# Performance work log

Hardware: AMD Instinct MI355X
Metric: run time of the kernel (lower is better)

The kernel has to match this reference:

```python
import jax, jax.numpy as jnp
import numpy as np

N_NOTES = 4096
SIZE = 64
N_EDGE_TYPE = 14  # len(GRAPH_KEYS) * 2
N_ITER = 5


def setup_inputs() -> dict:
    key = jax.random.key(0)
    ks = jax.random.split(key, 12)
    xav = np.sqrt(2.0 / (SIZE + SIZE))  # xavier_normal_ std for square [SIZE,SIZE]
    x = jax.random.normal(ks[0], (N_NOTES, SIZE), dtype=jnp.float32)
    # sparse binary adjacency per edge type (avg degree ~8) to keep gate
    # pre-activations in a sane range, as a real score graph would be
    edge_matrix = (jax.random.uniform(ks[1], (N_EDGE_TYPE, N_NOTES, N_NOTES)) < 0.002).astype(jnp.float32)
    wz = jax.random.normal(ks[2], (N_EDGE_TYPE, SIZE, SIZE), dtype=jnp.float32) * xav
    wr = jax.random.normal(ks[3], (N_EDGE_TYPE, SIZE, SIZE), dtype=jnp.float32) * xav
    wh = jax.random.normal(ks[4], (N_EDGE_TYPE, SIZE, SIZE), dtype=jnp.float32) * xav
    uz = jax.random.normal(ks[5], (SIZE, SIZE), dtype=jnp.float32) * xav
    ur = jax.random.normal(ks[6], (SIZE, SIZE), dtype=jnp.float32) * xav
    uh = jax.random.normal(ks[7], (SIZE, SIZE), dtype=jnp.float32) * xav
    bz = jnp.zeros((SIZE,), dtype=jnp.float32)
    br = jnp.zeros((SIZE,), dtype=jnp.float32)
    bh = jnp.zeros((SIZE,), dtype=jnp.float32)
    return {"x": x, "edge_matrix": edge_matrix, "wz": wz, "wr": wr, "wh": wh,
            "uz": uz, "ur": ur, "uh": uh, "bz": bz, "br": br, "bh": bh}


def reference(x, edge_matrix, wz, wr, wh, uz, ur, uh, bz, br, bh):
    # Faithful GatedGraph.forward: 5 iterations of edge-typed message passing
    # with GRU-style gates and the (unusual, but as-written) blend
    #   h <- (1 - z) * h + r * h_tilde
    h = x  # [N, D]
    for _ in range(N_ITER):
        # activation[e, n, d] = sum_m edge[e, m, n] * h[m, d]  (edge_matrix.transpose(1,2) @ h)
        act = jnp.einsum('emn,md->end', edge_matrix, h)  # [E, N, D]
        az = jnp.einsum('end,edf->nf', act, wz)  # bmm(act, wz).sum(0)
        ar = jnp.einsum('end,edf->nf', act, wr)
        ah = jnp.einsum('end,edf->nf', act, wh)
        z = jax.nn.sigmoid(az + h @ uz + bz)
        r = jax.nn.sigmoid(ar + h @ ur + br)
        h_tilde = jnp.tanh(ah + (r * h) @ uh + bh)
        h = (1.0 - z) * h + r * h_tilde
    return h
```

## Files before the change

kernel.cpp:

```cpp
#include <hip/hip_runtime.h>
#include <hip/hip_bf16.h>
#include <cstdint>

#define N_NOTES 4096
#define SIZE 64
#define NE 14
#define NITER 5
#define MAXDEG 64
#define KTOT 960
#define ASTR 968
#define HPAD 4113
#define PWN 184320
#define PUN 4096
#define PSTR 264

typedef __attribute__((ext_vector_type(8))) short short8;
typedef __attribute__((ext_vector_type(4))) float float4v;

__device__ __forceinline__ ushort f2bf(float f){
  union{float f; uint32_t u;} x; x.f=f;
  uint32_t r = x.u + 0x7fffu + ((x.u>>16)&1u);
  return (ushort)(r>>16);
}
__device__ __forceinline__ float bf2f(ushort h){
  union{uint32_t u; float f;} x; x.u=((uint32_t)h)<<16; return x.f;
}
__device__ __forceinline__ void split_bf(float v, ushort& hi, ushort& lo){
  hi = f2bf(v);
  lo = f2bf(v - bf2f(hi));
}

__global__ __launch_bounds__(256) void k_zero(int* __restrict__ deg, uint32_t* __restrict__ adj32,
                                              float* __restrict__ h0pad, float* __restrict__ h1pad){
  int i = blockIdx.x*256 + threadIdx.x;
  if (i < NE*N_NOTES) deg[i] = 0;
  for (int j = i; j < NE*N_NOTES*MAXDEG/2; j += gridDim.x*256)
    adj32[j] = 0x10101010u;
  if (i < (HPAD-N_NOTES)*SIZE){ h0pad[i] = 0.f; h1pad[i] = 0.f; }
}

__global__ __launch_bounds__(256) void k_build(const float4v* __restrict__ edge4,
                                               int* __restrict__ deg,
                                               ushort* __restrict__ adj){
  int row = blockIdx.x;
  int e = row >> 12, m = row & 4095;
  const float4v* p = edge4 + (size_t)row * (N_NOTES/4);
  int t = threadIdx.x;
  #pragma unroll
  for (int i=0;i<4;i++){
    int idx4 = t + i*256;
    float4v v = p[idx4];
    int nbase = idx4*4;
    #pragma unroll
    for (int j=0;j<4;j++){
      if (v[j] != 0.0f){
        int n = nbase + j;
        int slot = atomicAdd(&deg[(e<<12)+n], 1);
        if (slot < MAXDEG) adj[(size_t)((e<<12)+n)*MAXDEG + slot] = (ushort)m;
      }
    }
  }
}

__global__ __launch_bounds__(256) void k_pack(const float* __restrict__ wz, const float* __restrict__ wr,
                                              const float* __restrict__ wh, const float* __restrict__ uz,
                                              const float* __restrict__ ur, const float* __restrict__ uh,
                                              ushort* __restrict__ PWH, ushort* __restrict__ PWL,
                                              ushort* __restrict__ PUH, ushort* __restrict__ PUL){
  int idx = blockIdx.x*256 + threadIdx.x;
  if (idx < PWN){
    int j = idx & 7, lane = (idx>>3)&63, t = idx>>9;
    int kk = t % 30, wg = t/30; int cb = wg & 3, g = wg >> 2;
    int col = g*64 + cb*16 + (lane&15);
    int k = kk*32 + ((lane>>4)<<3) + j;
    int e = k >> 6, d = k & 63, f = col & 63;
    float v;
    if (e < NE){
      const float* wp = (g==0)?wz:(g==1)?wr:wh;
      v = wp[(e*64 + d)*64 + f];
    } else {
      v = (g==0) ? uz[d*64+f] : (g==1) ? ur[d*64+f] : 0.0f;
    }
    ushort hi,lo; split_bf(v,hi,lo);
    PWH[idx]=hi; PWL[idx]=lo;
  } else if (idx < PWN + PUN){
    int i2 = idx - PWN;
    int j = i2 & 7, lane = (i2>>3)&63, t = i2>>9;
    int kk = t & 1, cb = t >> 1;
    int col = cb*16 + (lane&15);
    int k = kk*32 + ((lane>>4)<<3) + j;
    float v = uh[k*64 + col];
    ushort hi,lo; split_bf(v,hi,lo);
    PUH[i2]=hi; PUL[i2]=lo;
  }
}

__global__ __launch_bounds__(1024, 4)
void k_fused(const int* __restrict__ deg, const ushort* __restrict__ adj,
             const ushort* __restrict__ PWH, const ushort* __restrict__ PWL,
             const ushort* __restrict__ PUH, const ushort* __restrict__ PUL,
             const float* __restrict__ bz, const float* __restrict__ br,
             const float* __restrict__ bh,
             const float* __restrict__ hin, float* __restrict__ hout,
             float* __restrict__ out, int last){
  __shared__ ushort sh[31744];
  ushort* aHs = sh;
  ushort* aLs = sh + 16*ASTR;
  float*  PSf = (float*)sh;
  ushort* rhH = sh + 25344;
  ushort* rhL = sh + 26496;
  float*  zSf = (float*)(sh + 27648);
  float*  rSf = (float*)(sh + 29696);

  const int tid  = threadIdx.x;
  const int w    = tid >> 6;
  const int lane = tid & 63;
  const int qi   = lane >> 4;
  const int ql   = lane & 15;
  const int l15  = lane & 15;
  const int koff = (lane >> 4) * 8;
  const int r0   = blockIdx.x * 16;
  const float4v* hin4 = (const float4v*)hin;

  const int Q = w*4 + qi;
  int dgv[4], mvv[4];
  #pragma unroll
  for (int p=0;p<4;p++){
    int u = p*64 + Q;
    int e = u >> 4, n = r0 + (u & 15);
    if (e < NE){
      int base = (e<<12) + n;
      dgv[p] = deg[base];
      mvv[p] = adj[(size_t)base*MAXDEG + ql];
    } else { dgv[p]=0; mvv[p]=0; }
  }
  #pragma unroll
  for (int p=0;p<4;p++){
    int u = p*64 + Q;
    if (u >= 240) continue;
    int e = u >> 4, ri = u & 15, n = r0 + ri;
    float4v a0={0.f,0.f,0.f,0.f}, a1={0.f,0.f,0.f,0.f};
    float4v a2={0.f,0.f,0.f,0.f}, a3={0.f,0.f,0.f,0.f};
    if (e < NE){
      #pragma unroll
      for (int k=0;k<16;k+=4){
        int m0 = __shfl(mvv[p], qi*16 + k);
        int m1 = __shfl(mvv[p], qi*16 + k+1);
        int m2 = __shfl(mvv[p], qi*16 + k+2);
        int m3 = __shfl(mvv[p], qi*16 + k+3);
        a0 += hin4[m0*16 + ql];
        a1 += hin4[m1*16 + ql];
        a2 += hin4[m2*16 + ql];
        a3 += hin4[m3*16 + ql];
      }
      int dg = dgv[p];
      if (dg > 16){
        size_t base = (size_t)((e<<12)+n)*MAXDEG;
        for (int k=16;k<dg;k++){
          int m = adj[base + k];
          a0 += hin4[m*16 + ql];
        }
      }
    } else {
      a0 = hin4[n*16 + ql];
    }
    float4v acc = (a0 + a1) + (a2 + a3);
    ushort h0,h1,h2,h3,l0,l1,l2,l3;
    split_bf(acc[0],h0,l0); split_bf(acc[1],h1,l1);
    split_bf(acc[2],h2,l2); split_bf(acc[3],h3,l3);
    int o = ri*ASTR + e*64 + ql*4;
    *(ushort4*)&aHs[o] = make_ushort4(h0,h1,h2,h3);
    *(ushort4*)&aLs[o] = make_ushort4(l0,l1,l2,l3);
  }
  __syncthreads();

  const int cb = w & 3, kq = w >> 2;
  const int kk0 = kq*8;
  float4v acc[3];
  #pragma unroll
  for (int g=0;g<3;g++) acc[g] = (float4v){0.f,0.f,0.f,0.f};
  #pragma unroll
  for (int kx=0; kx<8; ++kx){
    int kk = kk0 + kx;
    if (kk < 30){
      short8 aH = *(const short8*)&aHs[l15*ASTR + kk*32 + koff];
      short8 aL = *(const short8*)&aLs[l15*ASTR + kk*32 + koff];
      #pragma unroll
      for (int g=0; g<3; ++g){
        int boff = (((g*4 + cb)*30 + kk) << 9) + lane*8;
        short8 bH = *(const short8*)(PWH + boff);
        short8 bL = *(const short8*)(PWL + boff);
        acc[g] = __builtin_amdgcn_mfma_f32_16x16x32_bf16(aH,bH,acc[g],0,0,0);
        acc[g] = __builtin_amdgcn_mfma_f32_16x16x32_bf16(aH,bL,acc[g],0,0,0);
        acc[g] = __builtin_amdgcn_mfma_f32_16x16x32_bf16(aL,bH,acc[g],0,0,0);
      }
    }
  }
  __syncthreads();

  {
    int crow0 = (lane>>4)*4;
    #pragma unroll
    for (int g=0;g<3;g++){
      float* slot = PSf + (size_t)(kq*12 + g*4 + cb)*PSTR;
      #pragma unroll
      for (int i=0;i<4;i++)
        slot[(crow0+i)*16 + l15] = acc[g][i];
    }
  }
  __syncthreads();

  {
    int r = tid >> 6, f = tid & 63;
    int cb2 = f >> 4, c = f & 15;
    float az=0.f, ar=0.f, ah=0.f;
    #pragma unroll
    for (int k=0;k<4;k++){
      az += PSf[(size_t)(k*12 + 0 + cb2)*PSTR + r*16 + c];
      ar += PSf[(size_t)(k*12 + 4 + cb2)*PSTR + r*16 + c];
      ah += PSf[(size_t)(k*12 + 8 + cb2)*PSTR + r*16 + c];
    }
    float z = 1.f/(1.f + expf(-(az + bz[f])));
    float rg = 1.f/(1.f + expf(-(ar + br[f])));
    float hv = hin[(size_t)(r0+r)*64 + f];
    zSf[tid] = z;
    rSf[tid] = rg;
    ushort hi,lo; split_bf(rg*hv,hi,lo);
    rhH[r*72+f] = hi;
    rhL[r*72+f] = lo;
    PSf[(size_t)(8 + cb2)*PSTR + r*16 + c] = ah;
  }
  __syncthreads();

  if (w < 4){
    const int colf = w*16 + l15;
    float4v acc2 = {0.f,0.f,0.f,0.f};
    #pragma unroll
    for (int kk=0; kk<2; ++kk){
      short8 aH = *(const short8*)&rhH[l15*72 + kk*32 + koff];
      short8 aL = *(const short8*)&rhL[l15*72 + kk*32 + koff];
      int boff = (((w<<1) + kk) << 9) + lane*8;
      short8 bH = *(const short8*)(PUH + boff);
      short8 bL = *(const short8*)(PUL + boff);
      acc2 = __builtin_amdgcn_mfma_f32_16x16x32_bf16(aH,bH,acc2,0,0,0);
      acc2 = __builtin_amdgcn_mfma_f32_16x16x32_bf16(aH,bL,acc2,0,0,0);
      acc2 = __builtin_amdgcn_mfma_f32_16x16x32_bf16(aL,bH,acc2,0,0,0);
    }
    const int crow0 = (lane>>4)*4;
    const float bhf = bh[colf];
    #pragma unroll
    for (int i=0;i<4;i++){
      int row = crow0 + i;
      float ah = PSf[(size_t)(8 + w)*PSTR + row*16 + l15];
      float z  = zSf[row*64 + colf];
      float rg = rSf[row*64 + colf];
      float ht = tanhf(ah + acc2[i] + bhf);
      size_t idx = (size_t)(r0+row)*64 + colf;
      float hn = (1.f - z)*hin[idx] + rg*ht;
      hout[idx] = hn;
      if (last) out[idx] = hn;
    }
  }
}

extern "C" void kernel_launch(void* const* d_in, const int* in_sizes, int n_in,
                              void* d_out, int out_size, void* d_ws, size_t ws_size,
                              hipStream_t stream) {
  const float* x    = (const float*)d_in[0];
  const float* edge = (const float*)d_in[1];
  const float* wz   = (const float*)d_in[2];
  const float* wr   = (const float*)d_in[3];
  const float* wh   = (const float*)d_in[4];
  const float* uz   = (const float*)d_in[5];
  const float* ur   = (const float*)d_in[6];
  const float* uh   = (const float*)d_in[7];
  const float* bz   = (const float*)d_in[8];
  const float* br   = (const float*)d_in[9];
  const float* bh   = (const float*)d_in[10];
  float* out = (float*)d_out;

  char* ws = (char*)d_ws;
  size_t off = 0;
  auto alloc = [&](size_t bytes)->void*{
    void* p = ws + off;
    off = (off + bytes + 255) & ~(size_t)255;
    return p;
  };
  const size_t EN = (size_t)NE * N_NOTES;
  const size_t ND = (size_t)N_NOTES * SIZE;
  int*    deg  = (int*)   alloc(EN * 4);
  ushort* adj  = (ushort*)alloc(EN * MAXDEG * 2);
  ushort* PWH  = (ushort*)alloc((size_t)PWN * 2);
  ushort* PWL  = (ushort*)alloc((size_t)PWN * 2);
  ushort* PUH  = (ushort*)alloc((size_t)PUN * 2);
  ushort* PUL  = (ushort*)alloc((size_t)PUN * 2);
  float*  h0   = (float*) alloc((size_t)HPAD * SIZE * 4);
  float*  h1   = (float*) alloc((size_t)HPAD * SIZE * 4);

  k_zero <<<2048, 256, 0, stream>>>(deg, (uint32_t*)adj, h0 + ND, h1 + ND);
  k_build<<<NE*N_NOTES, 256, 0, stream>>>((const float4v*)edge, deg, adj);
  k_pack <<<(PWN + PUN)/256, 256, 0, stream>>>(wz, wr, wh, uz, ur, uh, PWH, PWL, PUH, PUL);
  hipMemcpyAsync(h0, x, ND*4, hipMemcpyDeviceToDevice, stream);

  float* hcur = h0;
  float* hnxt = h1;
  for (int it = 0; it < NITER; ++it){
    k_fused<<<N_NOTES/16, 1024, 0, stream>>>(deg, adj, PWH, PWL, PUH, PUL,
                                             bz, br, bh, hcur, hnxt,
                                             out, (it == NITER-1) ? 1 : 0);
    float* t = hcur; hcur = hnxt; hnxt = t;
  }
}
```

Before: 285.7 us.

## Warp-specialize fused kernel: producer warps gather per edge type, consumers run MFMA

Result: slower. 311.7 us (+9.1%).

```diff
diff --git a/kernel.cpp b/kernel.cpp
--- a/kernel.cpp
+++ b/kernel.cpp
@@ -8,11 +8,9 @@
 #define NITER 5
 #define MAXDEG 64
 #define KTOT 960
-#define ASTR 968
 #define HPAD 4113
 #define PWN 184320
 #define PUN 4096
-#define PSTR 264
 
 typedef __attribute__((ext_vector_type(8))) short short8;
 typedef __attribute__((ext_vector_type(4))) float float4v;
@@ -95,6 +93,36 @@
   }
 }
 
+__device__ __forceinline__ void gather_store(const float4v* __restrict__ hin4,
+                                             const ushort* __restrict__ adjRow,
+                                             int mv, int dg, int qi, int ql,
+                                             ushort* __restrict__ dH, ushort* __restrict__ dL){
+  float4v a0={0.f,0.f,0.f,0.f}, a1=a0, a2=a0, a3=a0;
+  #pragma unroll
+  for (int k=0;k<16;k+=4){
+    int m0 = __shfl(mv, qi*16 + k);
+    int m1 = __shfl(mv, qi*16 + k+1);
+    int m2 = __shfl(mv, qi*16 + k+2);
+    int m3 = __shfl(mv, qi*16 + k+3);
+    a0 += hin4[m0*16 + ql];
+    a1 += hin4[m1*16 + ql];
+    a2 += hin4[m2*16 + ql];
+    a3 += hin4[m3*16 + ql];
+  }
+  if (dg > 16){
+    for (int k=16;k<dg;k++){
+      int m = adjRow[k];
+      a0 += hin4[m*16 + ql];
+    }
+  }
+  float4v acc = (a0 + a1) + (a2 + a3);
+  ushort h0,h1,h2,h3,l0,l1,l2,l3;
+  split_bf(acc[0],h0,l0); split_bf(acc[1],h1,l1);
+  split_bf(acc[2],h2,l2); split_bf(acc[3],h3,l3);
+  *(ushort4*)dH = make_ushort4(h0,h1,h2,h3);
+  *(ushort4*)dL = make_ushort4(l0,l1,l2,l3);
+}
+
 __global__ __launch_bounds__(1024, 4)
 void k_fused(const int* __restrict__ deg, const ushort* __restrict__ adj,
              const ushort* __restrict__ PWH, const ushort* __restrict__ PWL,
@@ -103,132 +131,117 @@
              const float* __restrict__ bh,
              const float* __restrict__ hin, float* __restrict__ hout,
              float* __restrict__ out, int last){
-  __shared__ ushort sh[31744];
-  ushort* aHs = sh;
-  ushort* aLs = sh + 16*ASTR;
-  float*  PSf = (float*)sh;
-  ushort* rhH = sh + 25344;
-  ushort* rhL = sh + 26496;
-  float*  zSf = (float*)(sh + 27648);
-  float*  rSf = (float*)(sh + 29696);
+  __shared__ ushort AbH[2*16*72];
+  __shared__ ushort AbL[2*16*72];
+  __shared__ float  GSf[16*200];
+  __shared__ ushort rhHs[16*72];
+  __shared__ ushort rhLs[16*72];
+  __shared__ float  zSf[1024];
+  __shared__ float  rSf[1024];
 
   const int tid  = threadIdx.x;
   const int w    = tid >> 6;
   const int lane = tid & 63;
-  const int qi   = lane >> 4;
-  const int ql   = lane & 15;
   const int l15  = lane & 15;
   const int koff = (lane >> 4) * 8;
   const int r0   = blockIdx.x * 16;
   const float4v* hin4 = (const float4v*)hin;
 
-  const int Q = w*4 + qi;
-  int dgv[4], mvv[4];
+  const bool prod = (w >= 12);
+  const int qi = lane >> 4, ql = lane & 15;
+  const int cb = w & 3, g = w >> 2;
+
+  int dg_c=0, mv_c=0, dg_n=0, mv_n=0, n=0, ri=0;
+  if (prod){
+    ri = (w-12)*4 + qi;
+    n  = r0 + ri;
+    int dg0 = deg[n];
+    int mv0 = adj[(size_t)n*MAXDEG + ql];
+    int b1  = (1<<12) + n;
+    dg_c = deg[b1];
+    mv_c = adj[(size_t)b1*MAXDEG + ql];
+    if (dg0 > MAXDEG) dg0 = MAXDEG;
+    gather_store(hin4, adj + (size_t)n*MAXDEG, mv0, dg0, qi, ql,
+                 &AbH[ri*72 + ql*4], &AbL[ri*72 + ql*4]);
+  }
+
+  short8 cH0,cL0,cH1,cL1,nH0,nL0,nH1,nL1;
+  if (!prod){
+    int t0 = ((g*4+cb)*30) << 9;
+    cH0 = *(const short8*)(PWH + t0 + lane*8);
+    cL0 = *(const short8*)(PWL + t0 + lane*8);
+    cH1 = *(const short8*)(PWH + t0 + 512 + lane*8);
+    cL1 = *(const short8*)(PWL + t0 + 512 + lane*8);
+  }
+  __syncthreads();
+
+  float4v acc = {0.f,0.f,0.f,0.f};
   #pragma unroll
-  for (int p=0;p<4;p++){
-    int u = p*64 + Q;
-    int e = u >> 4, n = r0 + (u & 15);
-    if (e < NE){
-      int base = (e<<12) + n;
-      dgv[p] = deg[base];
-      mvv[p] = adj[(size_t)base*MAXDEG + ql];
-    } else { dgv[p]=0; mvv[p]=0; }
-  }
-  #pragma unroll
-  for (int p=0;p<4;p++){
-    int u = p*64 + Q;
-    if (u >= 240) continue;
-    int e = u >> 4, ri = u & 15, n = r0 + ri;
-    float4v a0={0.f,0.f,0.f,0.f}, a1={0.f,0.f,0.f,0.f};
-    float4v a2={0.f,0.f,0.f,0.f}, a3={0.f,0.f,0.f,0.f};
-    if (e < NE){
-      #pragma unroll
-      for (int k=0;k<16;k+=4){
-        int m0 = __shfl(mvv[p], qi*16 + k);
-        int m1 = __shfl(mvv[p], qi*16 + k+1);
-        int m2 = __shfl(mvv[p], qi*16 + k+2);
-        int m3 = __shfl(mvv[p], qi*16 + k+3);
-        a0 += hin4[m0*16 + ql];
-        a1 += hin4[m1*16 + ql];
-        a2 += hin4[m2*16 + ql];
-        a3 += hin4[m3*16 + ql];
+  for (int s=0; s<15; ++s){
+    if (prod){
+      if (s < 12){
+        int bn = ((s+2)<<12) + n;
+        dg_n = deg[bn];
+        mv_n = adj[(size_t)bn*MAXDEG + ql];
       }
-      int dg = dgv[p];
-      if (dg > 16){
-        size_t base = (size_t)((e<<12)+n)*MAXDEG;
-        for (int k=16;k<dg;k++){
-          int m = adj[base + k];
-          a0 += hin4[m*16 + ql];
-        }
+      if (s < 13){
+        int dgc = dg_c > MAXDEG ? MAXDEG : dg_c;
+        int bb = ((s+1)&1)*1152 + ri*72 + ql*4;
+        gather_store(hin4, adj + (size_t)(((s+1)<<12)+n)*MAXDEG, mv_c, dgc, qi, ql,
+                     &AbH[bb], &AbL[bb]);
+        dg_c = dg_n; mv_c = mv_n;
+      } else if (s == 13){
+        float4v av = hin4[n*16 + ql];
+        ushort h0,h1,h2,h3,l0,l1,l2,l3;
+        split_bf(av[0],h0,l0); split_bf(av[1],h1,l1);
+        split_bf(av[2],h2,l2); split_bf(av[3],h3,l3);
+        int bb = ri*72 + ql*4;
+        *(ushort4*)&AbH[bb] = make_ushort4(h0,h1,h2,h3);
+        *(ushort4*)&AbL[bb] = make_ushort4(l0,l1,l2,l3);
       }
     } else {
-      a0 = hin4[n*16 + ql];
-    }
-    float4v acc = (a0 + a1) + (a2 + a3);
-    ushort h0,h1,h2,h3,l0,l1,l2,l3;
-    split_bf(acc[0],h0,l0); split_bf(acc[1],h1,l1);
-    split_bf(acc[2],h2,l2); split_bf(acc[3],h3,l3);
-    int o = ri*ASTR + e*64 + ql*4;
-    *(ushort4*)&aHs[o] = make_ushort4(h0,h1,h2,h3);
-    *(ushort4*)&aLs[o] = make_ushort4(l0,l1,l2,l3);
+      if (s < 14){
+        int tn = ((g*4+cb)*30 + 2*(s+1)) << 9;
+        nH0 = *(const short8*)(PWH + tn + lane*8);
+        nL0 = *(const short8*)(PWL + tn + lane*8);
+        nH1 = *(const short8*)(PWH + tn + 512 + lane*8);
+        nL1 = *(const short8*)(PWL + tn + 512 + lane*8);
+      }
+      const int ab = (s&1)*1152 + l15*72;
+      short8 aH0 = *(const short8*)&AbH[ab + koff];
+      short8 aL0 = *(const short8*)&AbL[ab + koff];
+      short8 aH1 = *(const short8*)&AbH[ab + 32 + koff];
+      short8 aL1 = *(const short8*)&AbL[ab + 32 + koff];
+      acc = __builtin_amdgcn_mfma_f32_16x16x32_bf16(aH0,cH0,acc,0,0,0);
+      acc = __builtin_amdgcn_mfma_f32_16x16x32_bf16(aH0,cL0,acc,0,0,0);
+      acc = __builtin_amdgcn_mfma_f32_16x16x32_bf16(aL0,cH0,acc,0,0,0);
+      acc = __builtin_amdgcn_mfma_f32_16x16x32_bf16(aH1,cH1,acc,0,0,0);
+      acc = __builtin_amdgcn_mfma_f32_16x16x32_bf16(aH1,cL1,acc,0,0,0);
+      acc = __builtin_amdgcn_mfma_f32_16x16x32_bf16(aL1,cH1,acc,0,0,0);
+      if (s < 14){ cH0=nH0; cL0=nL0; cH1=nH1; cL1=nL1; }
+    }
+    __syncthreads();
+  }
+
+  if (!prod){
+    int crow0 = (lane>>4)*4;
+    int colg = g*64 + cb*16 + l15;
+    #pragma unroll
+    for (int i=0;i<4;i++)
+      GSf[(crow0+i)*200 + colg] = acc[i];
   }
   __syncthreads();
 
-  const int cb = w & 3, kq = w >> 2;
-  const int kk0 = kq*8;
-  float4v acc[3];
-  #pragma unroll
-  for (int g=0;g<3;g++) acc[g] = (float4v){0.f,0.f,0.f,0.f};
-  #pragma unroll
-  for (int kx=0; kx<8; ++kx){
-    int kk = kk0 + kx;
-    if (kk < 30){
-      short8 aH = *(const short8*)&aHs[l15*ASTR + kk*32 + koff];
-      short8 aL = *(const short8*)&aLs[l15*ASTR + kk*32 + koff];
-      #pragma unroll
-      for (int g=0; g<3; ++g){
-        int boff = (((g*4 + cb)*30 + kk) << 9) + lane*8;
-        short8 bH = *(const short8*)(PWH + boff);
-        short8 bL = *(const short8*)(PWL + boff);
-        acc[g] = __builtin_amdgcn_mfma_f32_16x16x32_bf16(aH,bH,acc[g],0,0,0);
-        acc[g] = __builtin_amdgcn_mfma_f32_16x16x32_bf16(aH,bL,acc[g],0,0,0);
-        acc[g] = __builtin_amdgcn_mfma_f32_16x16x32_bf16(aL,bH,acc[g],0,0,0);
-      }
-    }
-  }
-  __syncthreads();
-
   {
-    int crow0 = (lane>>4)*4;
-    #pragma unroll
-    for (int g=0;g<3;g++){
-      float* slot = PSf + (size_t)(kq*12 + g*4 + cb)*PSTR;
-      #pragma unroll
-      for (int i=0;i<4;i++)
-        slot[(crow0+i)*16 + l15] = acc[g][i];
-    }
-  }
-  __syncthreads();
-
-  {
-    int r = tid >> 6, f = tid & 63;
-    int cb2 = f >> 4, c = f & 15;
-    float az=0.f, ar=0.f, ah=0.f;
-    #pragma unroll
-    for (int k=0;k<4;k++){
-      az += PSf[(size_t)(k*12 + 0 + cb2)*PSTR + r*16 + c];
-      ar += PSf[(size_t)(k*12 + 4 + cb2)*PSTR + r*16 + c];
-      ah += PSf[(size_t)(k*12 + 8 + cb2)*PSTR + r*16 + c];
-    }
-    float z = 1.f/(1.f + expf(-(az + bz[f])));
+    int rr = tid >> 6, f = tid & 63;
+    float az = GSf[rr*200 + f];
+    float ar = GSf[rr*200 + 64 + f];
+    float z  = 1.f/(1.f + expf(-(az + bz[f])));
     float rg = 1.f/(1.f + expf(-(ar + br[f])));
-    float hv = hin[(size_t)(r0+r)*64 + f];
-    zSf[tid] = z;
-    rSf[tid] = rg;
+    float hv = hin[(size_t)(r0+rr)*64 + f];
+    zSf[tid] = z; rSf[tid] = rg;
     ushort hi,lo; split_bf(rg*hv,hi,lo);
-    rhH[r*72+f] = hi;
-    rhL[r*72+f] = lo;
-    PSf[(size_t)(8 + cb2)*PSTR + r*16 + c] = ah;
+    rhHs[rr*72+f] = hi; rhLs[rr*72+f] = lo;
   }
   __syncthreads();
 
@@ -237,8 +250,8 @@
     float4v acc2 = {0.f,0.f,0.f,0.f};
     #pragma unroll
     for (int kk=0; kk<2; ++kk){
-      short8 aH = *(const short8*)&rhH[l15*72 + kk*32 + koff];
-      short8 aL = *(const short8*)&rhL[l15*72 + kk*32 + koff];
+      short8 aH = *(const short8*)&rhHs[l15*72 + kk*32 + koff];
+      short8 aL = *(const short8*)&rhLs[l15*72 + kk*32 + koff];
       int boff = (((w<<1) + kk) << 9) + lane*8;
       short8 bH = *(const short8*)(PUH + boff);
       short8 bL = *(const short8*)(PUL + boff);
@@ -251,7 +264,7 @@
     #pragma unroll
     for (int i=0;i<4;i++){
       int row = crow0 + i;
-      float ah = PSf[(size_t)(8 + w)*PSTR + row*16 + l15];
+      float ah = GSf[row*200 + 128 + colf];
       float z  = zSf[row*64 + colf];
       float rg = rSf[row*64 + colf];
       float ht = tanhf(ah + acc2[i] + bhf);
```

## Overlap neighbor gather with MFMA phase by staging gather across wave groups

Applied to the files above, without the earlier changes.

New measurement: 305.6 us (median of 2 runs). +7.0%, slower.

```diff
diff --git a/kernel.cpp b/kernel.cpp
--- a/kernel.cpp
+++ b/kernel.cpp
@@ -95,6 +95,46 @@
   }
 }
 
+__device__ __forceinline__ void gather_unit(const float4v* __restrict__ hin4,
+                                            const int* __restrict__ deg,
+                                            const ushort* __restrict__ adj,
+                                            int e, int n, int qi, int ql,
+                                            ushort* __restrict__ dH, ushort* __restrict__ dL){
+  float4v acc;
+  if (e < NE){
+    int base = (e<<12) + n;
+    int dg = deg[base]; if (dg > MAXDEG) dg = MAXDEG;
+    int mv = adj[(size_t)base*MAXDEG + ql];
+    float4v a0={0.f,0.f,0.f,0.f}, a1=a0, a2=a0, a3=a0;
+    #pragma unroll
+    for (int k=0;k<16;k+=4){
+      int m0 = __shfl(mv, qi*16 + k);
+      int m1 = __shfl(mv, qi*16 + k+1);
+      int m2 = __shfl(mv, qi*16 + k+2);
+      int m3 = __shfl(mv, qi*16 + k+3);
+      a0 += hin4[m0*16 + ql];
+      a1 += hin4[m1*16 + ql];
+      a2 += hin4[m2*16 + ql];
+      a3 += hin4[m3*16 + ql];
+    }
+    if (dg > 16){
+      const ushort* arow = adj + (size_t)base*MAXDEG;
+      for (int k=16;k<dg;k++){
+        int m = arow[k];
+        a0 += hin4[m*16 + ql];
+      }
+    }
+    acc = (a0 + a1) + (a2 + a3);
+  } else {
+    acc = hin4[n*16 + ql];
+  }
+  ushort h0,h1,h2,h3,l0,l1,l2,l3;
+  split_bf(acc[0],h0,l0); split_bf(acc[1],h1,l1);
+  split_bf(acc[2],h2,l2); split_bf(acc[3],h3,l3);
+  *(ushort4*)dH = make_ushort4(h0,h1,h2,h3);
+  *(ushort4*)dL = make_ushort4(l0,l1,l2,l3);
+}
+
 __global__ __launch_bounds__(1024, 4)
 void k_fused(const int* __restrict__ deg, const ushort* __restrict__ adj,
              const ushort* __restrict__ PWH, const ushort* __restrict__ PWL,
@@ -119,84 +159,57 @@
   const int ql   = lane & 15;
   const int l15  = lane & 15;
   const int koff = (lane >> 4) * 8;
+  const int cb   = w & 3, kq = w >> 2;
   const int r0   = blockIdx.x * 16;
   const float4v* hin4 = (const float4v*)hin;
 
-  const int Q = w*4 + qi;
-  int dgv[4], mvv[4];
-  #pragma unroll
-  for (int p=0;p<4;p++){
-    int u = p*64 + Q;
-    int e = u >> 4, n = r0 + (u & 15);
-    if (e < NE){
-      int base = (e<<12) + n;
-      dgv[p] = deg[base];
-      mvv[p] = adj[(size_t)base*MAXDEG + ql];
-    } else { dgv[p]=0; mvv[p]=0; }
-  }
-  #pragma unroll
-  for (int p=0;p<4;p++){
-    int u = p*64 + Q;
-    if (u >= 240) continue;
-    int e = u >> 4, ri = u & 15, n = r0 + ri;
-    float4v a0={0.f,0.f,0.f,0.f}, a1={0.f,0.f,0.f,0.f};
-    float4v a2={0.f,0.f,0.f,0.f}, a3={0.f,0.f,0.f,0.f};
-    if (e < NE){
-      #pragma unroll
-      for (int k=0;k<16;k+=4){
-        int m0 = __shfl(mvv[p], qi*16 + k);
-        int m1 = __shfl(mvv[p], qi*16 + k+1);
-        int m2 = __shfl(mvv[p], qi*16 + k+2);
-        int m3 = __shfl(mvv[p], qi*16 + k+3);
-        a0 += hin4[m0*16 + ql];
-        a1 += hin4[m1*16 + ql];
-        a2 += hin4[m2*16 + ql];
-        a3 += hin4[m3*16 + ql];
-      }
-      int dg = dgv[p];
-      if (dg > 16){
-        size_t base = (size_t)((e<<12)+n)*MAXDEG;
-        for (int k=16;k<dg;k++){
-          int m = adj[base + k];
-          a0 += hin4[m*16 + ql];
-        }
-      }
-    } else {
-      a0 = hin4[n*16 + ql];
-    }
-    float4v acc = (a0 + a1) + (a2 + a3);
-    ushort h0,h1,h2,h3,l0,l1,l2,l3;
-    split_bf(acc[0],h0,l0); split_bf(acc[1],h1,l1);
-    split_bf(acc[2],h2,l2); split_bf(acc[3],h3,l3);
-    int o = ri*ASTR + e*64 + ql*4;
-    *(ushort4*)&aHs[o] = make_ushort4(h0,h1,h2,h3);
-    *(ushort4*)&aLs[o] = make_ushort4(l0,l1,l2,l3);
+  {
+    int u = w*4 + qi, e = u >> 4, ri = u & 15;
+    gather_unit(hin4, deg, adj, e, r0+ri, qi, ql,
+                &aHs[ri*ASTR + e*64 + ql*4], &aLs[ri*ASTR + e*64 + ql*4]);
   }
   __syncthreads();
 
-  const int cb = w & 3, kq = w >> 2;
-  const int kk0 = kq*8;
   float4v acc[3];
   #pragma unroll
   for (int g=0;g<3;g++) acc[g] = (float4v){0.f,0.f,0.f,0.f};
+
   #pragma unroll
-  for (int kx=0; kx<8; ++kx){
-    int kk = kk0 + kx;
-    if (kk < 30){
-      short8 aH = *(const short8*)&aHs[l15*ASTR + kk*32 + koff];
-      short8 aL = *(const short8*)&aLs[l15*ASTR + kk*32 + koff];
+  for (int p=1; p<=4; ++p){
+    if (kq == p-1){
+      const int kk0 = (p-1)*8;
       #pragma unroll
-      for (int g=0; g<3; ++g){
-        int boff = (((g*4 + cb)*30 + kk) << 9) + lane*8;
-        short8 bH = *(const short8*)(PWH + boff);
-        short8 bL = *(const short8*)(PWL + boff);
-        acc[g] = __builtin_amdgcn_mfma_f32_16x16x32_bf16(aH,bH,acc[g],0,0,0);
-        acc[g] = __builtin_amdgcn_mfma_f32_16x16x32_bf16(aH,bL,acc[g],0,0,0);
-        acc[g] = __builtin_amdgcn_mfma_f32_16x16x32_bf16(aL,bH,acc[g],0,0,0);
+      for (int kx=0; kx<8; ++kx){
+        const int kk = kk0 + kx;
+        if (kk < 30){
+          short8 aH = *(const short8*)&aHs[l15*ASTR + kk*32 + koff];
+          short8 aL = *(const short8*)&aLs[l15*ASTR + kk*32 + koff];
+          #pragma unroll
+          for (int g=0; g<3; ++g){
+            int boff = (((g*4 + cb)*30 + kk) << 9) + lane*8;
+            short8 bH = *(const short8*)(PWH + boff);
+            short8 bL = *(const short8*)(PWL + boff);
+            acc[g] = __builtin_amdgcn_mfma_f32_16x16x32_bf16(aH,bH,acc[g],0,0,0);
+            acc[g] = __builtin_amdgcn_mfma_f32_16x16x32_bf16(aH,bL,acc[g],0,0,0);
+            acc[g] = __builtin_amdgcn_mfma_f32_16x16x32_bf16(aL,bH,acc[g],0,0,0);
+          }
+        }
       }
-    }
-  }
-  __syncthreads();
+    } else if (p <= 3){
+      int widx = w - ((kq > p-1) ? 4 : 0);
+      int u = p*64 + widx*4 + qi;
+      int e = u >> 4, ri = u & 15;
+      gather_unit(hin4, deg, adj, e, r0+ri, qi, ql,
+                  &aHs[ri*ASTR + e*64 + ql*4], &aLs[ri*ASTR + e*64 + ql*4]);
+      if (p < 3 && widx < 4){
+        int u2 = p*64 + 48 + widx*4 + qi;
+        int e2 = u2 >> 4, ri2 = u2 & 15;
+        gather_unit(hin4, deg, adj, e2, r0+ri2, qi, ql,
+                    &aHs[ri2*ASTR + e2*64 + ql*4], &aLs[ri2*ASTR + e2*64 + ql*4]);
+      }
+    }
+    __syncthreads();
+  }
 
   {
     int crow0 = (lane>>4)*4;
```

## Merge iterations into persistent kernel with grid barrier and fuse setup kernels

Applied to the files above, without the earlier changes.

Result: slower. 507.1 us (+77.5%).

```diff
diff --git a/kernel.cpp b/kernel.cpp
--- a/kernel.cpp
+++ b/kernel.cpp
@@ -7,12 +7,12 @@
 #define NE 14
 #define NITER 5
 #define MAXDEG 64
-#define KTOT 960
 #define ASTR 968
 #define HPAD 4113
 #define PWN 184320
 #define PUN 4096
 #define PSTR 264
+#define NBLK 256
 
 typedef __attribute__((ext_vector_type(8))) short short8;
 typedef __attribute__((ext_vector_type(4))) float float4v;
@@ -30,12 +30,46 @@
   lo = f2bf(v - bf2f(hi));
 }
 
-__global__ __launch_bounds__(256) void k_zero(int* __restrict__ deg, uint32_t* __restrict__ adj32,
-                                              float* __restrict__ h0pad, float* __restrict__ h1pad){
+__global__ __launch_bounds__(256) void k_setup(int* __restrict__ deg, uint32_t* __restrict__ adj32,
+                                               const float* __restrict__ wz, const float* __restrict__ wr,
+                                               const float* __restrict__ wh, const float* __restrict__ uz,
+                                               const float* __restrict__ ur, const float* __restrict__ uh,
+                                               ushort* __restrict__ PWH, ushort* __restrict__ PWL,
+                                               ushort* __restrict__ PUH, ushort* __restrict__ PUL,
+                                               const float4v* __restrict__ x4, float4v* __restrict__ h04,
+                                               float* __restrict__ h0pad, float* __restrict__ h1pad,
+                                               int* __restrict__ bar){
   int i = blockIdx.x*256 + threadIdx.x;
+  if (i == 0) bar[0] = 0;
   if (i < NE*N_NOTES) deg[i] = 0;
-  for (int j = i; j < NE*N_NOTES*MAXDEG/2; j += gridDim.x*256)
+  for (int j = i; j < NE*N_NOTES*MAXDEG/2; j += 2048*256)
     adj32[j] = 0x10101010u;
+  if (i < PWN){
+    int j = i & 7, lane = (i>>3)&63, t = i>>9;
+    int kk = t % 30, wg = t/30; int cb = wg & 3, g = wg >> 2;
+    int col = g*64 + cb*16 + (lane&15);
+    int k = kk*32 + ((lane>>4)<<3) + j;
+    int e = k >> 6, d = k & 63, f = col & 63;
+    float v;
+    if (e < NE){
+      const float* wp = (g==0)?wz:(g==1)?wr:wh;
+      v = wp[(e*64 + d)*64 + f];
+    } else {
+      v = (g==0) ? uz[d*64+f] : (g==1) ? ur[d*64+f] : 0.0f;
+    }
+    ushort hi,lo; split_bf(v,hi,lo);
+    PWH[i]=hi; PWL[i]=lo;
+  } else if (i < PWN + PUN){
+    int i2 = i - PWN;
+    int j = i2 & 7, lane = (i2>>3)&63, t = i2>>9;
+    int kk = t & 1, cb = t >> 1;
+    int col = cb*16 + (lane&15);
+    int k = kk*32 + ((lane>>4)<<3) + j;
+    float v = uh[k*64 + col];
+    ushort hi,lo; split_bf(v,hi,lo);
+    PUH[i2]=hi; PUL[i2]=lo;
+  }
+  if (i < N_NOTES*SIZE/4) h04[i] = x4[i];
   if (i < (HPAD-N_NOTES)*SIZE){ h0pad[i] = 0.f; h1pad[i] = 0.f; }
 }
 
@@ -62,47 +96,14 @@
   }
 }
 
-__global__ __launch_bounds__(256) void k_pack(const float* __restrict__ wz, const float* __restrict__ wr,
-                                              const float* __restrict__ wh, const float* __restrict__ uz,
-                                              const float* __restrict__ ur, const float* __restrict__ uh,
-                                              ushort* __restrict__ PWH, ushort* __restrict__ PWL,
-                                              ushort* __restrict__ PUH, ushort* __restrict__ PUL){
-  int idx = blockIdx.x*256 + threadIdx.x;
-  if (idx < PWN){
-    int j = idx & 7, lane = (idx>>3)&63, t = idx>>9;
-    int kk = t % 30, wg = t/30; int cb = wg & 3, g = wg >> 2;
-    int col = g*64 + cb*16 + (lane&15);
-    int k = kk*32 + ((lane>>4)<<3) + j;
-    int e = k >> 6, d = k & 63, f = col & 63;
-    float v;
-    if (e < NE){
-      const float* wp = (g==0)?wz:(g==1)?wr:wh;
-      v = wp[(e*64 + d)*64 + f];
-    } else {
-      v = (g==0) ? uz[d*64+f] : (g==1) ? ur[d*64+f] : 0.0f;
-    }
-    ushort hi,lo; split_bf(v,hi,lo);
-    PWH[idx]=hi; PWL[idx]=lo;
-  } else if (idx < PWN + PUN){
-    int i2 = idx - PWN;
-    int j = i2 & 7, lane = (i2>>3)&63, t = i2>>9;
-    int kk = t & 1, cb = t >> 1;
-    int col = cb*16 + (lane&15);
-    int k = kk*32 + ((lane>>4)<<3) + j;
-    float v = uh[k*64 + col];
-    ushort hi,lo; split_bf(v,hi,lo);
-    PUH[i2]=hi; PUL[i2]=lo;
-  }
-}
-
 __global__ __launch_bounds__(1024, 4)
-void k_fused(const int* __restrict__ deg, const ushort* __restrict__ adj,
-             const ushort* __restrict__ PWH, const ushort* __restrict__ PWL,
-             const ushort* __restrict__ PUH, const ushort* __restrict__ PUL,
-             const float* __restrict__ bz, const float* __restrict__ br,
-             const float* __restrict__ bh,
-             const float* __restrict__ hin, float* __restrict__ hout,
-             float* __restrict__ out, int last){
+void k_mega(const int* __restrict__ deg, const ushort* __restrict__ adj,
+            const ushort* __restrict__ PWH, const ushort* __restrict__ PWL,
+            const ushort* __restrict__ PUH, const ushort* __restrict__ PUL,
+            const float* __restrict__ bz, const float* __restrict__ br,
+            const float* __restrict__ bh,
+            float* __restrict__ h0, float* __restrict__ h1,
+            float* __restrict__ out, int* __restrict__ bar){
   __shared__ ushort sh[31744];
   ushort* aHs = sh;
   ushort* aLs = sh + 16*ASTR;
@@ -119,146 +120,171 @@
   const int ql   = lane & 15;
   const int l15  = lane & 15;
   const int koff = (lane >> 4) * 8;
+  const int cb   = w & 3, kq = w >> 2;
   const int r0   = blockIdx.x * 16;
-  const float4v* hin4 = (const float4v*)hin;
-
-  const int Q = w*4 + qi;
+  const int Q    = w*4 + qi;
+
   int dgv[4], mvv[4];
   #pragma unroll
   for (int p=0;p<4;p++){
     int u = p*64 + Q;
-    int e = u >> 4, n = r0 + (u & 15);
-    if (e < NE){
-      int base = (e<<12) + n;
-      dgv[p] = deg[base];
-      mvv[p] = adj[(size_t)base*MAXDEG + ql];
-    } else { dgv[p]=0; mvv[p]=0; }
+    dgv[p]=0; mvv[p]=0;
+    if (u < 240){
+      int e = u >> 4;
+      if (e < NE){
+        int base = (e<<12) + r0 + (u & 15);
+        int d = deg[base]; if (d > MAXDEG) d = MAXDEG;
+        dgv[p] = d;
+        mvv[p] = adj[(size_t)base*MAXDEG + ql];
+      }
+    }
   }
-  #pragma unroll
-  for (int p=0;p<4;p++){
-    int u = p*64 + Q;
-    if (u >= 240) continue;
-    int e = u >> 4, ri = u & 15, n = r0 + ri;
-    float4v a0={0.f,0.f,0.f,0.f}, a1={0.f,0.f,0.f,0.f};
-    float4v a2={0.f,0.f,0.f,0.f}, a3={0.f,0.f,0.f,0.f};
-    if (e < NE){
-      #pragma unroll
-      for (int k=0;k<16;k+=4){
-        int m0 = __shfl(mvv[p], qi*16 + k);
-        int m1 = __shfl(mvv[p], qi*16 + k+1);
-        int m2 = __shfl(mvv[p], qi*16 + k+2);
-        int m3 = __shfl(mvv[p], qi*16 + k+3);
-        a0 += hin4[m0*16 + ql];
-        a1 += hin4[m1*16 + ql];
-        a2 += hin4[m2*16 + ql];
-        a3 += hin4[m3*16 + ql];
-      }
-      int dg = dgv[p];
-      if (dg > 16){
-        size_t base = (size_t)((e<<12)+n)*MAXDEG;
-        for (int k=16;k<dg;k++){
-          int m = adj[base + k];
-          a0 += hin4[m*16 + ql];
+
+  #pragma unroll 1
+  for (int it = 0; it < NITER; ++it){
+    const float* hin  = (it & 1) ? h1 : h0;
+    float*       hout = (it & 1) ? h0 : h1;
+    const float4v* hin4 = (const float4v*)hin;
+
+    #pragma unroll
+    for (int p=0;p<4;p++){
+      int u = p*64 + Q;
+      if (u >= 240) continue;
+      int e = u >> 4, ri = u & 15, n = r0 + ri;
+      float4v a0={0.f,0.f,0.f,0.f}, a1=a0, a2=a0, a3=a0;
+      if (e < NE){
+        int mv = mvv[p];
+        #pragma unroll
+        for (int k=0;k<16;k+=4){
+          int m0 = __shfl(mv, qi*16 + k);
+          int m1 = __shfl(mv, qi*16 + k+1);
+          int m2 = __shfl(mv, qi*16 + k+2);
+          int m3 = __shfl(mv, qi*16 + k+3);
+          a0 += hin4[m0*16 + ql];
+          a1 += hin4[m1*16 + ql];
+          a2 += hin4[m2*16 + ql];
+          a3 += hin4[m3*16 + ql];
         }
-      }
-    } else {
-      a0 = hin4[n*16 + ql];
-    }
-    float4v acc = (a0 + a1) + (a2 + a3);
-    ushort h0,h1,h2,h3,l0,l1,l2,l3;
-    split_bf(acc[0],h0,l0); split_bf(acc[1],h1,l1);
-    split_bf(acc[2],h2,l2); split_bf(acc[3],h3,l3);
-    int o = ri*ASTR + e*64 + ql*4;
-    *(ushort4*)&aHs[o] = make_ushort4(h0,h1,h2,h3);
-    *(ushort4*)&aLs[o] = make_ushort4(l0,l1,l2,l3);
-  }
-  __syncthreads();
-
-  const int cb = w & 3, kq = w >> 2;
-  const int kk0 = kq*8;
-  float4v acc[3];
-  #pragma unroll
-  for (int g=0;g<3;g++) acc[g] = (float4v){0.f,0.f,0.f,0.f};
-  #pragma unroll
-  for (int kx=0; kx<8; ++kx){
-    int kk = kk0 + kx;
-    if (kk < 30){
-      short8 aH = *(const short8*)&aHs[l15*ASTR + kk*32 + koff];
-      short8 aL = *(const short8*)&aLs[l15*ASTR + kk*32 + koff];
-      #pragma unroll
-      for (int g=0; g<3; ++g){
-        int boff = (((g*4 + cb)*30 + kk) << 9) + lane*8;
-        short8 bH = *(const short8*)(PWH + boff);
-        short8 bL = *(const short8*)(PWL + boff);
-        acc[g] = __builtin_amdgcn_mfma_f32_16x16x32_bf16(aH,bH,acc[g],0,0,0);
-        acc[g] = __builtin_amdgcn_mfma_f32_16x16x32_bf16(aH,bL,acc[g],0,0,0);
-        acc[g] = __builtin_amdgcn_mfma_f32_16x16x32_bf16(aL,bH,acc[g],0,0,0);
-      }
-    }
-  }
-  __syncthreads();
-
-  {
-    int crow0 = (lane>>4)*4;
+        int dg = dgv[p];
+        if (dg > 16){
+          size_t base = (size_t)((e<<12)+n)*MAXDEG;
+          for (int k=16;k<dg;k++){
+            int m = adj[base + k];
+            a0 += hin4[m*16 + ql];
+          }
+        }
+      } else {
+        a0 = hin4[n*16 + ql];
+      }
+      float4v acc = (a0 + a1) + (a2 + a3);
+      ushort h0_,h1_,h2_,h3_,l0_,l1_,l2_,l3_;
+      split_bf(acc[0],h0_,l0_); split_bf(acc[1],h1_,l1_);
+      split_bf(acc[2],h2_,l2_); split_bf(acc[3],h3_,l3_);
+      int o = ri*ASTR + e*64 + ql*4;
+      *(ushort4*)&aHs[o] = make_ushort4(h0_,h1_,h2_,h3_);
+      *(ushort4*)&aLs[o] = make_ushort4(l0_,l1_,l2_,l3_);
+    }
+    __syncthreads();
+
+    float4v acc[3];
     #pragma unroll
-    for (int g=0;g<3;g++){
-      float* slot = PSf + (size_t)(kq*12 + g*4 + cb)*PSTR;
-      #pragma unroll
-      for (int i=0;i<4;i++)
-        slot[(crow0+i)*16 + l15] = acc[g][i];
-    }
-  }
-  __syncthreads();
-
-  {
-    int r = tid >> 6, f = tid & 63;
-    int cb2 = f >> 4, c = f & 15;
-    float az=0.f, ar=0.f, ah=0.f;
-    #pragma unroll
-    for (int k=0;k<4;k++){
-      az += PSf[(size_t)(k*12 + 0 + cb2)*PSTR + r*16 + c];
-      ar += PSf[(size_t)(k*12 + 4 + cb2)*PSTR + r*16 + c];
-      ah += PSf[(size_t)(k*12 + 8 + cb2)*PSTR + r*16 + c];
-    }
-    float z = 1.f/(1.f + expf(-(az + bz[f])));
-    float rg = 1.f/(1.f + expf(-(ar + br[f])));
-    float hv = hin[(size_t)(r0+r)*64 + f];
-    zSf[tid] = z;
-    rSf[tid] = rg;
-    ushort hi,lo; split_bf(rg*hv,hi,lo);
-    rhH[r*72+f] = hi;
-    rhL[r*72+f] = lo;
-    PSf[(size_t)(8 + cb2)*PSTR + r*16 + c] = ah;
-  }
-  __syncthreads();
-
-  if (w < 4){
-    const int colf = w*16 + l15;
-    float4v acc2 = {0.f,0.f,0.f,0.f};
-    #pragma unroll
-    for (int kk=0; kk<2; ++kk){
-      short8 aH = *(const short8*)&rhH[l15*72 + kk*32 + koff];
-      short8 aL = *(const short8*)&rhL[l15*72 + kk*32 + koff];
-      int boff = (((w<<1) + kk) << 9) + lane*8;
-      short8 bH = *(const short8*)(PUH + boff);
-      short8 bL = *(const short8*)(PUL + boff);
-      acc2 = __builtin_amdgcn_mfma_f32_16x16x32_bf16(aH,bH,acc2,0,0,0);
-      acc2 = __builtin_amdgcn_mfma_f32_16x16x32_bf16(aH,bL,acc2,0,0,0);
-      acc2 = __builtin_amdgcn_mfma_f32_16x16x32_bf16(aL,bH,acc2,0,0,0);
-    }
-    const int crow0 = (lane>>4)*4;
-    const float bhf = bh[colf];
-    #pragma unroll
-    for (int i=0;i<4;i++){
-      int row = crow0 + i;
-      float ah = PSf[(size_t)(8 + w)*PSTR + row*16 + l15];
-      float z  = zSf[row*64 + colf];
-      float rg = rSf[row*64 + colf];
-      float ht = tanhf(ah + acc2[i] + bhf);
-      size_t idx = (size_t)(r0+row)*64 + colf;
-      float hn = (1.f - z)*hin[idx] + rg*ht;
-      hout[idx] = hn;
-      if (last) out[idx] = hn;
+    for (int g=0;g<3;g++) acc[g] = (float4v){0.f,0.f,0.f,0.f};
+    {
+      const int kk0 = kq*8;
+      #pragma unroll
+      for (int kx=0; kx<8; ++kx){
+        const int kk = kk0 + kx;
+        if (kk < 30){
+          short8 aH = *(const short8*)&aHs[l15*ASTR + kk*32 + koff];
+          short8 aL = *(const short8*)&aLs[l15*ASTR + kk*32 + koff];
+          #pragma unroll
+          for (int g=0; g<3; ++g){
+            int boff = (((g*4 + cb)*30 + kk) << 9) + lane*8;
+            short8 bH = *(const short8*)(PWH + boff);
+            short8 bL = *(const short8*)(PWL + boff);
+            acc[g] = __builtin_amdgcn_mfma_f32_16x16x32_bf16(aH,bH,acc[g],0,0,0);
+            acc[g] = __builtin_amdgcn_mfma_f32_16x16x32_bf16(aH,bL,acc[g],0,0,0);
+            acc[g] = __builtin_amdgcn_mfma_f32_16x16x32_bf16(aL,bH,acc[g],0,0,0);
+          }
+        }
+      }
+    }
+    __syncthreads();
+
+    {
+      int crow0 = (lane>>4)*4;
+      #pragma unroll
+      for (int g=0;g<3;g++){
+        float* slot = PSf + (size_t)(kq*12 + g*4 + cb)*PSTR;
+        #pragma unroll
+        for (int i=0;i<4;i++)
+          slot[(crow0+i)*16 + l15] = acc[g][i];
+      }
+    }
+    __syncthreads();
+
+    {
+      int r = tid >> 6, f = tid & 63;
+      int cb2 = f >> 4, c = f & 15;
+      float az=0.f, ar=0.f, ah=0.f;
+      #pragma unroll
+      for (int k=0;k<4;k++){
+        az += PSf[(size_t)(k*12 + 0 + cb2)*PSTR + r*16 + c];
+        ar += PSf[(size_t)(k*12 + 4 + cb2)*PSTR + r*16 + c];
+        ah += PSf[(size_t)(k*12 + 8 + cb2)*PSTR + r*16 + c];
+      }
+      float z  = 1.f/(1.f + expf(-(az + bz[f])));
+      float rg = 1.f/(1.f + expf(-(ar + br[f])));
+      float hv = hin[(size_t)(r0+r)*64 + f];
+      zSf[tid] = z;
+      rSf[tid] = rg;
+      ushort hi,lo; split_bf(rg*hv,hi,lo);
+      rhH[r*72+f] = hi;
+      rhL[r*72+f] = lo;
+      PSf[(size_t)(8 + cb2)*PSTR + r*16 + c] = ah;
+    }
+    __syncthreads();
+
+    if (w < 4){
+      const int colf = w*16 + l15;
+      float4v acc2 = {0.f,0.f,0.f,0.f};
+      #pragma unroll
+      for (int kk=0; kk<2; ++kk){
+        short8 aH = *(const short8*)&rhH[l15*72 + kk*32 + koff];
+        short8 aL = *(const short8*)&rhL[l15*72 + kk*32 + koff];
+        int boff = (((w<<1) + kk) << 9) + lane*8;
+        short8 bH = *(const short8*)(PUH + boff);
+        short8 bL = *(const short8*)(PUL + boff);
+        acc2 = __builtin_amdgcn_mfma_f32_16x16x32_bf16(aH,bH,acc2,0,0,0);
+        acc2 = __builtin_amdgcn_mfma_f32_16x16x32_bf16(aH,bL,acc2,0,0,0);
+        acc2 = __builtin_amdgcn_mfma_f32_16x16x32_bf16(aL,bH,acc2,0,0,0);
+      }
+      const int crow0 = (lane>>4)*4;
+      const float bhf = bh[colf];
+      #pragma unroll
+      for (int i=0;i<4;i++){
+        int row = crow0 + i;
+        float ah = PSf[(size_t)(8 + w)*PSTR + row*16 + l15];
+        float z  = zSf[row*64 + colf];
+        float rg = rSf[row*64 + colf];
+        float ht = tanhf(ah + acc2[i] + bhf);
+        size_t idx = (size_t)(r0+row)*64 + colf;
+        float hn = (1.f - z)*hin[idx] + rg*ht;
+        hout[idx] = hn;
+        if (it == NITER-1) out[idx] = hn;
+      }
+    }
+
+    if (it < NITER-1){
+      __syncthreads();
+      if (tid == 0){
+        __threadfence();
+        atomicAdd(bar, 1);
+        int target = NBLK * (it + 1);
+        while (atomicAdd(bar, 0) < target) __builtin_amdgcn_s_sleep(2);
+        __threadfence();
+      }
+      __syncthreads();
     }
   }
 }
@@ -296,18 +322,14 @@
   ushort* PUL  = (ushort*)alloc((size_t)PUN * 2);
   float*  h0   = (float*) alloc((size_t)HPAD * SIZE * 4);
   float*  h1   = (float*) alloc((size_t)HPAD * SIZE * 4);
-
-  k_zero <<<2048, 256, 0, stream>>>(deg, (uint32_t*)adj, h0 + ND, h1 + ND);
+  int*    bar  = (int*)   alloc(256);
+
+  k_setup<<<2048, 256, 0, stream>>>(deg, (uint32_t*)adj,
+                                    wz, wr, wh, uz, ur, uh,
+                                    PWH, PWL, PUH, PUL,
+                                    (const float4v*)x, (float4v*)h0,
+                                    h0 + ND, h1 + ND, bar);
   k_build<<<NE*N_NOTES, 256, 0, stream>>>((const float4v*)edge, deg, adj);
-  k_pack <<<(PWN + PUN)/256, 256, 0, stream>>>(wz, wr, wh, uz, ur, uh, PWH, PWL, PUH, PUL);
-  hipMemcpyAsync(h0, x, ND*4, hipMemcpyDeviceToDevice, stream);
-
-  float* hcur = h0;
-  float* hnxt = h1;
-  for (int it = 0; it < NITER; ++it){
-    k_fused<<<N_NOTES/16, 1024, 0, stream>>>(deg, adj, PWH, PWL, PUH, PUL,
-                                             bz, br, bh, hcur, hnxt,
-                                             out, (it == NITER-1) ? 1 : 0);
-    float* t = hcur; hcur = hnxt; hnxt = t;
-  }
-}
+  k_mega <<<NBLK, 1024, 0, stream>>>(deg, adj, PWH, PWL, PUH, PUL,
+                                     bz, br, bh, h0, h1, out, bar);
+}
```
